# Kernel tuning notes

Hardware: AMD Instinct MI355X
Metric: run time of the kernel (lower is better)

## Reference

```python
import jax, jax.numpy as jnp
import numpy as np

N = 8192
E = 262144
IN_DIM = 128
OUT_DIM = 16


def _linear_params(key, fan_in, fan_out):
    k1, k2 = jax.random.split(key)
    bound = 1.0 / np.sqrt(fan_in)
    W = jax.random.uniform(k1, (fan_in, fan_out), jnp.float32, -bound, bound)
    b = jax.random.uniform(k2, (fan_out,), jnp.float32, -bound, bound)
    return W, b


def setup_inputs() -> dict:
    key = jax.random.key(0)
    ks = jax.random.split(key, 10)
    x = jax.random.normal(ks[0], (N, IN_DIM), jnp.float32)
    edge_index = jax.random.randint(ks[1], (2, E), 0, N, jnp.int64)
    W1, b1 = _linear_params(ks[2], IN_DIM, 128)
    W2, b2 = _linear_params(ks[3], 128, 256)
    W3, b3 = _linear_params(ks[4], 256, 64)
    Wk, bk = _linear_params(ks[5], 256, 256)
    Wq, bq = _linear_params(ks[6], 256, 256)
    Wr, br = _linear_params(ks[7], IN_DIM, 64)
    Wf, bf = _linear_params(ks[8], 64, OUT_DIM)
    ln_g = jnp.ones((64,), jnp.float32)
    ln_b = jnp.zeros((64,), jnp.float32)
    return dict(x=x, edge_index=edge_index, W1=W1, b1=b1, W2=W2, b2=b2,
                W3=W3, b3=b3, Wk=Wk, bk=bk, Wq=Wq, bq=bq, Wr=Wr, br=br,
                ln_g=ln_g, ln_b=ln_b, Wf=Wf, bf=bf)


def gcn_conv(x, W, b, row, col, n):
    # PyG GCNConv: add self-loops, symmetric normalization, aggregate src->dst
    xw = x @ W                                          # [N, F_out]
    loops = jnp.arange(n, dtype=row.dtype)
    r = jnp.concatenate([row, loops])
    c = jnp.concatenate([col, loops])
    deg = jax.ops.segment_sum(jnp.ones_like(c, jnp.float32), c, num_segments=n)
    dinv = jnp.where(deg > 0, jax.lax.rsqrt(jnp.maximum(deg, 1e-12)), 0.0)
    norm = dinv[r] * dinv[c]                            # [E+N]
    out = jax.ops.segment_sum(norm[:, None] * xw[r], c, num_segments=n)
    return out + b


def _forward(x, edge_index, W1, b1, W2, b2, W3, b3, Wk, bk, Wq, bq,
             Wr, br, ln_g, ln_b, Wf, bf):
    row, col = edge_index[0], edge_index[1]
    n = x.shape[0]
    residual = x @ Wr + br                              # [N, 64]
    h = jax.nn.leaky_relu(gcn_conv(x, W1, b1, row, col, n))   # dropout = eval no-op
    h = jax.nn.leaky_relu(gcn_conv(h, W2, b2, row, col, n))   # [N, 256]
    keys = h @ Wk + bk
    queries = h @ Wq + bq
    scores = queries @ keys.T                           # [N, N] dense, as in source
    mask = jnp.zeros((n, n), jnp.float32).at[row, col].set(1.0)
    scores = scores * mask                              # multiplicative mask (faithful)
    attn = jax.nn.softmax(scores, axis=-1)
    h = attn @ h                                        # [N, 256]
    h = jax.nn.leaky_relu(gcn_conv(h, W3, b3, row, col, n))   # [N, 64]
    z = h + residual
    mu = jnp.mean(z, axis=-1, keepdims=True)
    var = jnp.mean((z - mu) ** 2, axis=-1, keepdims=True)
    z = (z - mu) * jax.lax.rsqrt(var + 1e-5) * ln_g + ln_b
    pooled = jnp.max(z, axis=0)                         # 'max' pooling -> [64]
    return pooled @ Wf + bf                             # [OUT_DIM]


def reference(x, edge_index, W1, b1, W2, b2, W3, b3, Wk, bk, Wq, bq,
              Wr, br, ln_g, ln_b, Wf, bf):
    return _forward(x, edge_index, W1, b1, W2, b2, W3, b3, Wk, bk, Wq, bq,
                    Wr, br, ln_g, ln_b, Wf, bf)
```

## Files before the change

kernel.cpp:

```cpp
#include <hip/hip_runtime.h>
#include <hip/hip_fp16.h>
#include <cstdint>
#include <cstddef>

#define NNODES 8192
#define NEDGES 262144
#define MAXDEG 96
#define SMEM_BYTES 10496

typedef _Float16 f16x8 __attribute__((ext_vector_type(8)));
typedef _Float16 h2v   __attribute__((ext_vector_type(2)));
typedef float    f32x4 __attribute__((ext_vector_type(4)));

__device__ __forceinline__ float leaky(float v){ return v > 0.f ? v : 0.01f*v; }

__device__ __forceinline__ unsigned fmap(float f){
  unsigned u = __float_as_uint(f);
  return (u & 0x80000000u) ? ~u : (u | 0x80000000u);
}
__device__ __forceinline__ float funmap(unsigned u){
  return (u & 0x80000000u) ? __uint_as_float(u & 0x7FFFFFFFu) : __uint_as_float(~u);
}
__device__ __forceinline__ h2v as_h2(unsigned u){
  union{ unsigned x; h2v h; } c; c.x = u; return c.h;
}

struct GP {
  const float *x; const int *ei;
  const float *W1,*b1,*W2,*b2,*W3,*b3,*Wk,*bk,*Wq,*bq,*Wr,*br,*lng,*lnb,*Wf,*bfv;
  float* out;
  __half *xh,*xw1h,*h1h,*h1ah,*h2h,*qth,*gh,*hw3h;
  float *resid,*sw3;
  __half *Wqh,*Wkh,*Wqkt,*Wrt,*W1t,*W2t,*W3t;
  float *bqk,*wb,*s0p;
  int *degc,*degr,*csrc,*csrd;
  unsigned* poolpart;
};

__device__ __forceinline__ void pre_unit(const GP& p, int b, char* smem){
  int t = threadIdx.x;
  if (b < 1024){
    int base = (b*256 + t)*4;
    float4 xv = *(const float4*)(p.x + base);
    uint2 o;
    *(__half2*)&o.x = __floats2half2_rn(xv.x, xv.y);
    *(__half2*)&o.y = __floats2half2_rn(xv.z, xv.w);
    *(uint2*)(p.xh + base) = o;
  } else if (b < 1088){
    int base = ((b-1024)*256 + t)*4;
    float4 v = *(const float4*)(p.Wq + base);
    uint2 o;
    *(__half2*)&o.x = __floats2half2_rn(v.x, v.y);
    *(__half2*)&o.y = __floats2half2_rn(v.z, v.w);
    *(uint2*)(p.Wqh + base) = o;
  } else if (b < 1152){
    int base = ((b-1088)*256 + t)*4;
    float4 v = *(const float4*)(p.Wk + base);
    uint2 o;
    *(__half2*)&o.x = __floats2half2_rn(v.x, v.y);
    *(__half2*)&o.y = __floats2half2_rn(v.z, v.w);
    *(uint2*)(p.Wkh + base) = o;
  } else if (b < 1184){
    int idx = (b-1152)*256 + t;
    int nn = idx >> 7, k = idx & 127;
    p.Wrt[idx] = __float2half(p.Wr[k*64 + nn]);
  } else if (b < 1248){
    int idx = (b-1184)*256 + t;
    int nn = idx >> 7, k = idx & 127;
    p.W1t[idx] = __float2half(p.W1[k*128 + nn]);
  } else if (b < 1376){
    int idx = (b-1248)*256 + t;
    int nn = idx >> 7, k = idx & 127;
    p.W2t[idx] = __float2half(p.W2[k*256 + nn]);
  } else if (b < 1440){
    int idx = (b-1376)*256 + t;
    int nn = idx >> 8, k = idx & 255;
    p.W3t[idx] = __float2half(p.W3[k*64 + nn]);
  } else if (b < 1504){
    int idx = (b-1440)*256 + t;
    if (idx < 8192) p.degc[idx]=0; else p.degr[idx-8192]=0;
  } else if (b < 1520){
    p.poolpart[(b-1504)*256 + t] = 0u;
  } else if (b == 1520){
    if (t < 64) p.sw3[t]=0.f;
  } else {
    int c = b - 1521;
    float* ra = (float*)smem; float* rb = ra + 256; float* rc = rb + 256;
    ra[t] = p.Wk[c*256 + t] * p.bq[t];
    rb[t] = p.Wq[c*256 + t] * p.bk[t];
    if (c == 0) rc[t] = p.bq[t]*p.bk[t];
    __syncthreads();
    for (int off=128; off; off>>=1){
      if (t < off){
        ra[t] += ra[t+off];
        rb[t] += rb[t+off];
        if (c == 0) rc[t] += rc[t+off];
      }
      __syncthreads();
    }
    if (t == 0){
      p.bqk[c] = ra[0];
      p.wb[c]  = rb[0];
      if (c == 0) p.s0p[0] = rc[0];
    }
  }
}

__device__ __forceinline__ void gemm_tile(const __half* __restrict__ A,
    const __half* __restrict__ Bt, const float* __restrict__ bias,
    float* __restrict__ Cf, __half* __restrict__ Ch, float* __restrict__ csum,
    int K, int N, int act, int bx, int by,
    _Float16 (*As)[40], _Float16 (*Bs)[40], float* cs){
  int t = threadIdx.x, w = t>>6, lane = t&63;
  int m0 = bx*64, n0 = by*64;
  int quad = lane>>4, l15 = lane&15;
  int srow = t>>2, soff = (t&3)*8;
  f32x4 acc0 = {0.f,0.f,0.f,0.f}, acc1 = acc0, acc2 = acc0, acc3 = acc0;
  for (int k0 = 0; k0 < K; k0 += 32){
    *(uint4*)&As[srow][soff] = *(const uint4*)(A  + (size_t)(m0+srow)*K + k0 + soff);
    *(uint4*)&Bs[srow][soff] = *(const uint4*)(Bt + (size_t)(n0+srow)*K + k0 + soff);
    __syncthreads();
    f16x8 af = *(const f16x8*)&As[w*16 + l15][quad*8];
    f16x8 b0 = *(const f16x8*)&Bs[ 0 + l15][quad*8];
    f16x8 b1 = *(const f16x8*)&Bs[16 + l15][quad*8];
    f16x8 b2 = *(const f16x8*)&Bs[32 + l15][quad*8];
    f16x8 b3 = *(const f16x8*)&Bs[48 + l15][quad*8];
    acc0 = __builtin_amdgcn_mfma_f32_16x16x32_f16(af, b0, acc0, 0,0,0);
    acc1 = __builtin_amdgcn_mfma_f32_16x16x32_f16(af, b1, acc1, 0,0,0);
    acc2 = __builtin_amdgcn_mfma_f32_16x16x32_f16(af, b2, acc2, 0,0,0);
    acc3 = __builtin_amdgcn_mfma_f32_16x16x32_f16(af, b3, acc3, 0,0,0);
    __syncthreads();
  }
  f32x4 accs[4] = {acc0, acc1, acc2, acc3};
  if (csum){
    if (t < 64) cs[t] = 0.f;
    __syncthreads();
    #pragma unroll
    for (int nt=0; nt<4; ++nt){
      float pp = accs[nt][0]+accs[nt][1]+accs[nt][2]+accs[nt][3];
      atomicAdd(&cs[nt*16 + l15], pp);
    }
    __syncthreads();
    if (t < 64) atomicAdd(&csum[n0 + t], cs[t]);
  }
  #pragma unroll
  for (int nt=0; nt<4; ++nt){
    int col = n0 + nt*16 + l15;
    float bv = bias ? bias[col] : 0.f;
    #pragma unroll
    for (int r=0;r<4;r++){
      int row = m0 + w*16 + quad*4 + r;
      float v = accs[nt][r] + bv;
      if (act) v = leaky(v);
      if (Cf) Cf[(size_t)row*N + col] = v;
      if (Ch) Ch[(size_t)row*N + col] = __float2half(v);
    }
  }
}

template<int INS, int OUTS, int ACT>
__device__ __forceinline__ void agg128w(const __half* __restrict__ in,
    const int* __restrict__ deg, const int* __restrict__ src,
    __half* __restrict__ outp, const float* __restrict__ bias, int i){
  int lane = threadIdx.x & 63;
  int dcc = deg[i];
  float dc = rsqrtf((float)(dcc+1));
  int e0 = i*MAXDEG, e1 = e0 + dcc;
  float2 acc = make_float2(0.f, 0.f);
  for (int eb = e0; eb < e1; eb += 8){
    int m = e1 - eb; if (m > 8) m = 8;
    int r[8];
    #pragma unroll
    for (int u=0;u<8;u++) r[u] = src[(u<m) ? eb+u : eb];
    __half2 hv[8]; float sc[8];
    #pragma unroll
    for (int u=0;u<8;u++){
      hv[u] = *(const __half2*)(in + (size_t)r[u]*128 + lane*2);
      sc[u] = INS ? 1.f : rsqrtf((float)(deg[r[u]]+1));
    }
    #pragma unroll
    for (int u=0;u<8;u++){
      if (u < m){
        float2 h = __half22float2(hv[u]);
        if (INS){ acc.x += h.x; acc.y += h.y; }
        else { acc.x = fmaf(sc[u], h.x, acc.x); acc.y = fmaf(sc[u], h.y, acc.y); }
      }
    }
  }
  float2 self = __half22float2(*(const __half2*)(in + (size_t)i*128 + lane*2));
  float ss = INS ? 1.f : dc;
  float ox = dc*(ss*self.x + acc.x);
  float oy = dc*(ss*self.y + acc.y);
  if (ACT){
    ox = leaky(ox + bias[lane*2]);
    oy = leaky(oy + bias[lane*2+1]);
  }
  if (OUTS){ ox *= dc; oy *= dc; }
  *(__half2*)(outp + (size_t)i*128 + lane*2) = __floats2half2_rn(ox, oy);
}

__device__ __forceinline__ void attn_unit(const GP& p, int u){
  const int n = NNODES;
  int w = threadIdx.x>>6, lane = threadIdx.x&63;
  int i = u*4 + w;
  int fo = lane*4;
  uint2 qtu = *(const uint2*)(p.qth + (size_t)i*256 + fo);
  h2v q0 = as_h2(qtu.x), q1 = as_h2(qtu.y);
  float4 wbv = *(const float4*)(p.wb + fo);
  uint2 hiu  = *(const uint2*)(p.h2h + (size_t)i*256 + fo);
  float2 hia = __half22float2(*(__half2*)&hiu.x);
  float2 hib = __half22float2(*(__half2*)&hiu.y);
  float pv = hia.x*wbv.x + hia.y*wbv.y + hib.x*wbv.z + hib.y*wbv.w;
  #pragma unroll
  for (int mm=32; mm; mm>>=1) pv += __shfl_xor(pv, mm, 64);
  float Ei = __expf(pv + p.s0p[0]);
  int dri = p.degr[i];
  int e0 = i*MAXDEG, e1 = e0 + dri;
  float acc = 0.f, dsum = 0.f;
  for (int eb = e0; eb < e1; eb += 8){
    int m = e1 - eb; if (m > 8) m = 8;
    int j[8];
    #pragma unroll
    for (int u8=0;u8<8;u8++) j[u8] = p.csrd[(u8<m) ? eb+u8 : eb];
    uint2 hv[8]; float gv[8];
    #pragma unroll
    for (int u8=0;u8<8;u8++){
      hv[u8] = *(const uint2*)(p.h2h + (size_t)j[u8]*256 + fo);
      gv[u8] = __half2float(p.gh[(size_t)j[u8]*64 + lane]);
    }
    float d[8];
    #pragma unroll
    for (int u8=0;u8<8;u8++)
      d[u8] = __builtin_amdgcn_fdot2(q1, as_h2(hv[u8].y),
              __builtin_amdgcn_fdot2(q0, as_h2(hv[u8].x), 0.f, false), false);
    #pragma unroll
    for (int mm=32; mm; mm>>=1){
      #pragma unroll
      for (int u8=0;u8<8;u8++) d[u8] += __shfl_xor(d[u8], mm, 64);
    }
    #pragma unroll
    for (int u8=0;u8<8;u8++){
      if (u8 < m){
        float we = Ei * __expf(d[u8]);
        dsum += we;
        acc = fmaf(we - 1.f, gv[u8], acc);
      }
    }
  }
  float inv = 1.0f / ((float)(n - dri) + dsum);
  float di = rsqrtf((float)(p.degc[i]+1));
  p.hw3h[(size_t)i*64 + lane] = __float2half(di * (p.sw3[lane] + acc) * inv);
}

__device__ __forceinline__ void zp_wave(const GP& p, int c){
  int lane = threadIdx.x & 63;
  int dcc = p.degc[c];
  float dc = rsqrtf((float)(dcc+1));
  float acc = 0.f;
  int e0 = c*MAXDEG, e1 = e0 + dcc;
  for (int eb = e0; eb < e1; eb += 8){
    int m = e1 - eb; if (m > 8) m = 8;
    int r[8];
    #pragma unroll
    for (int u=0;u<8;u++) r[u] = p.csrc[(u<m) ? eb+u : eb];
    __half hval[8];
    #pragma unroll
    for (int u=0;u<8;u++) hval[u] = p.hw3h[(size_t)r[u]*64 + lane];
    #pragma unroll
    for (int u=0;u<8;u++)
      if (u < m) acc += __half2float(hval[u]);
  }
  float self = __half2float(p.hw3h[(size_t)c*64 + lane]);
  float v = leaky(dc*(self + acc) + p.b3[lane]) + p.resid[(size_t)c*64 + lane];
  float s = v;
  #pragma unroll
  for (int mm=32; mm; mm>>=1) s += __shfl_xor(s, mm, 64);
  float mu = s * (1.0f/64.0f);
  float d = v - mu;
  float s2 = d*d;
  #pragma unroll
  for (int mm=32; mm; mm>>=1) s2 += __shfl_xor(s2, mm, 64);
  float zv = d * rsqrtf(s2*(1.0f/64.0f) + 1e-5f) * p.lng[lane] + p.lnb[lane];
  atomicMax(&p.poolpart[(c & 63)*64 + lane], fmap(zv));
}

__device__ __forceinline__ void final_unit(const GP& p, char* smem){
  int t = threadIdx.x, f = t & 63, g = t >> 6;
  unsigned (*sm)[64] = (unsigned(*)[64])smem;
  float* pool = (float*)(smem + 1024);
  unsigned mu = 0u;
  for (int b = g; b < 64; b += 4) mu = max(mu, p.poolpart[b*64 + f]);
  sm[g][f] = mu;
  __syncthreads();
  if (g == 0)
    pool[f] = funmap(max(max(sm[0][f],sm[1][f]), max(sm[2][f],sm[3][f])));
  __syncthreads();
  if (t < 16){
    float a = p.bfv[t];
    #pragma unroll
    for (int ff=0; ff<64; ++ff) a = fmaf(pool[ff], p.Wf[ff*16 + t], a);
    p.out[t] = a;
  }
}

__global__ __launch_bounds__(256) void k_pre(GP p){
  __shared__ __align__(16) char smem[SMEM_BYTES];
  pre_unit(p, blockIdx.x, smem);
}

__global__ __launch_bounds__(256) void k_sc(GP p){
  __shared__ __align__(16) char smem[SMEM_BYTES];
  _Float16 (*As)[40] = (_Float16(*)[40])smem;
  _Float16 (*Bs)[40] = (_Float16(*)[40])(smem + 5120);
  int b = blockIdx.x;
  if (b < 1024){
    int e = b*256 + threadIdx.x;
    int r = p.ei[e], c = p.ei[NEDGES+e];
    int p1 = atomicAdd(&p.degc[c],1); p.csrc[c*MAXDEG + p1] = r;
    int p2 = atomicAdd(&p.degr[r],1); p.csrd[r*MAXDEG + p2] = c;
  } else if (b < 1280){
    int bb = b - 1024;
    gemm_tile(p.xh, p.W1t, nullptr, nullptr, p.xw1h, nullptr, 128, 128, 0, bb>>1, bb&1, As, Bs, nullptr);
  } else if (b < 1296){
    int bb = b - 1280;
    gemm_tile(p.Wkh, p.Wqh, nullptr, nullptr, p.Wqkt, nullptr, 256, 256, 0, bb&3, bb>>2, As, Bs, nullptr);
  } else {
    gemm_tile(p.xh, p.Wrt, p.br, p.resid, nullptr, nullptr, 128, 64, 0, b-1296, 0, As, Bs, nullptr);
  }
}

__global__ __launch_bounds__(256) void k_agg0(GP p){
  int i = blockIdx.x*4 + (threadIdx.x>>6);
  agg128w<0,1,1>(p.xw1h, p.degc, p.csrc, p.h1h, p.b1, i);
}
__global__ __launch_bounds__(256) void k_agg1(GP p){
  int i = blockIdx.x*4 + (threadIdx.x>>6);
  agg128w<1,0,0>(p.h1h, p.degc, p.csrc, p.h1ah, nullptr, i);
}

__global__ __launch_bounds__(256) void k_gemm2(GP p){
  __shared__ __align__(16) char smem[SMEM_BYTES];
  _Float16 (*As)[40] = (_Float16(*)[40])smem;
  _Float16 (*Bs)[40] = (_Float16(*)[40])(smem + 5120);
  int b = blockIdx.x;
  gemm_tile(p.h1ah, p.W2t, p.b2, nullptr, p.h2h, nullptr, 128, 256, 1, b>>2, b&3, As, Bs, nullptr);
}

__global__ __launch_bounds__(256) void k_mix2(GP p){
  __shared__ __align__(16) char smem[SMEM_BYTES];
  _Float16 (*As)[40] = (_Float16(*)[40])smem;
  _Float16 (*Bs)[40] = (_Float16(*)[40])(smem + 5120);
  float* cs = (float*)(smem + 10240);
  int b = blockIdx.x;
  if (b < 128) gemm_tile(p.h2h, p.W3t, nullptr, nullptr, p.gh, p.sw3, 256, 64, 0, b, 0, As, Bs, cs);
  else {
    int bb = b - 128;
    gemm_tile(p.h2h, p.Wqkt, p.bqk, nullptr, p.qth, nullptr, 256, 256, 0, bb>>2, bb&3, As, Bs, cs);
  }
}

__global__ __launch_bounds__(256) void k_attn(GP p){ attn_unit(p, blockIdx.x); }

__global__ __launch_bounds__(256) void k_zp(GP p){
  int c = blockIdx.x*4 + (threadIdx.x>>6);
  zp_wave(p, c);
}

__global__ __launch_bounds__(256) void k_final(GP p){
  __shared__ __align__(16) char smem[SMEM_BYTES];
  final_unit(p, smem);
}

extern "C" void kernel_launch(void* const* d_in, const int* in_sizes, int n_in,
                              void* d_out, int out_size, void* d_ws, size_t ws_size,
                              hipStream_t stream){
  const int n = NNODES, E = NEDGES;
  char* ws = (char*)d_ws; size_t off = 0;
  auto alloc = [&](size_t bytes)->void*{
    void* pp = ws + off; off += (bytes + 255) & ~(size_t)255; return pp;
  };
  GP p;
  p.x   = (const float*)d_in[0];
  p.ei  = (const int*)d_in[1];
  p.W1  = (const float*)d_in[2];  p.b1 = (const float*)d_in[3];
  p.W2  = (const float*)d_in[4];  p.b2 = (const float*)d_in[5];
  p.W3  = (const float*)d_in[6];  p.b3 = (const float*)d_in[7];
  p.Wk  = (const float*)d_in[8];  p.bk = (const float*)d_in[9];
  p.Wq  = (const float*)d_in[10]; p.bq = (const float*)d_in[11];
  p.Wr  = (const float*)d_in[12]; p.br = (const float*)d_in[13];
  p.lng = (const float*)d_in[14]; p.lnb = (const float*)d_in[15];
  p.Wf  = (const float*)d_in[16]; p.bfv = (const float*)d_in[17];
  p.out = (float*)d_out;

  p.xh   = (__half*)alloc((size_t)n*128*2);
  p.xw1h = (__half*)alloc((size_t)n*128*2);
  p.h1h  = (__half*)alloc((size_t)n*128*2);
  p.h1ah = (__half*)alloc((size_t)n*128*2);
  p.h2h  = (__half*)alloc((size_t)n*256*2);
  p.qth  = (__half*)alloc((size_t)n*256*2);
  p.gh   = (__half*)alloc((size_t)n*64*2);
  p.hw3h = (__half*)alloc((size_t)n*64*2);
  p.resid= (float*)alloc((size_t)n*64*4);
  p.sw3  = (float*)alloc(64*4);
  p.Wqh  = (__half*)alloc(256*256*2);
  p.Wkh  = (__half*)alloc(256*256*2);
  p.Wqkt = (__half*)alloc(256*256*2);
  p.Wrt  = (__half*)alloc(128*64*2);
  p.W1t  = (__half*)alloc(128*128*2);
  p.W2t  = (__half*)alloc(128*256*2);
  p.W3t  = (__half*)alloc(256*64*2);
  p.bqk  = (float*)alloc(256*4);
  p.wb   = (float*)alloc(256*4);
  p.s0p  = (float*)alloc(4);
  p.degc = (int*)alloc((size_t)n*4);
  p.degr = (int*)alloc((size_t)n*4);
  p.csrc = (int*)alloc((size_t)n*MAXDEG*4);
  p.csrd = (int*)alloc((size_t)n*MAXDEG*4);
  p.poolpart = (unsigned*)alloc(64*64*4);

  k_pre  <<<dim3(1777), 256, 0, stream>>>(p);
  k_sc   <<<dim3(1424), 256, 0, stream>>>(p);
  k_agg0 <<<dim3(n/4),  256, 0, stream>>>(p);
  k_agg1 <<<dim3(n/4),  256, 0, stream>>>(p);
  k_gemm2<<<dim3(512),  256, 0, stream>>>(p);
  k_mix2 <<<dim3(640),  256, 0, stream>>>(p);
  k_attn <<<dim3(n/4),  256, 0, stream>>>(p);
  k_zp   <<<dim3(n/4),  256, 0, stream>>>(p);
  k_final<<<dim3(1),    256, 0, stream>>>(p);
}
```

Baseline: 216.7 us.

## Fuse final pooling into zp kernel via last-block counter; transpose attention reductions

Removes the separate single-block final kernel launch by having the last-finishing block of the zp kernel, detected with an atomic done counter, run the pooling and output projection. It reads pool partials via atomics for coherence. The attention edge loop now uses a butterfly transpose reduction, so each lane ends up holding one edge's score and computes a single exp instead of eight. The weights are then broadcast with shuffles. This trades fewer shuffles and exps for extra select logic and a fence-plus-atomic per block.

```diff
diff --git a/kernel.cpp b/kernel.cpp
--- a/kernel.cpp
+++ b/kernel.cpp
@@ -34,7 +34,7 @@
   __half *Wqh,*Wkh,*Wqkt,*Wrt,*W1t,*W2t,*W3t;
   float *bqk,*wb,*s0p;
   int *degc,*degr,*csrc,*csrd;
-  unsigned* poolpart;
+  unsigned* poolpart; unsigned* donecnt;
 };
 
 __device__ __forceinline__ void pre_unit(const GP& p, int b, char* smem){
@@ -83,6 +83,7 @@
     p.poolpart[(b-1504)*256 + t] = 0u;
   } else if (b == 1520){
     if (t < 64) p.sw3[t]=0.f;
+    else if (t == 64) *p.donecnt = 0u;
   } else {
     int c = b - 1521;
     float* ra = (float*)smem; float* rb = ra + 256; float* rc = rb + 256;
@@ -213,10 +214,11 @@
   float pv = hia.x*wbv.x + hia.y*wbv.y + hib.x*wbv.z + hib.y*wbv.w;
   #pragma unroll
   for (int mm=32; mm; mm>>=1) pv += __shfl_xor(pv, mm, 64);
-  float Ei = __expf(pv + p.s0p[0]);
+  float base = pv + p.s0p[0];
   int dri = p.degr[i];
   int e0 = i*MAXDEG, e1 = e0 + dri;
   float acc = 0.f, dsum = 0.f;
+  int slot = lane & 7;
   for (int eb = e0; eb < e1; eb += 8){
     int m = e1 - eb; if (m > 8) m = 8;
     int j[8];
@@ -234,16 +236,31 @@
       d[u8] = __builtin_amdgcn_fdot2(q1, as_h2(hv[u8].y),
               __builtin_amdgcn_fdot2(q0, as_h2(hv[u8].x), 0.f, false), false);
     #pragma unroll
-    for (int mm=32; mm; mm>>=1){
-      #pragma unroll
-      for (int u8=0;u8<8;u8++) d[u8] += __shfl_xor(d[u8], mm, 64);
-    }
+    for (int v=0;v<8;v++) d[v] += __shfl_xor(d[v], 1, 64);
+    float e0_ = (lane&1) ? d[1] : d[0];
+    float e1_ = (lane&1) ? d[3] : d[2];
+    float e2_ = (lane&1) ? d[5] : d[4];
+    float e3_ = (lane&1) ? d[7] : d[6];
+    e0_ += __shfl_xor(e0_, 2, 64);  e1_ += __shfl_xor(e1_, 2, 64);
+    e2_ += __shfl_xor(e2_, 2, 64);  e3_ += __shfl_xor(e3_, 2, 64);
+    float f0_ = (lane&2) ? e1_ : e0_;
+    float f1_ = (lane&2) ? e3_ : e2_;
+    f0_ += __shfl_xor(f0_, 4, 64);  f1_ += __shfl_xor(f1_, 4, 64);
+    float g_ = (lane&4) ? f1_ : f0_;
+    g_ += __shfl_xor(g_,  8, 64);
+    g_ += __shfl_xor(g_, 16, 64);
+    g_ += __shfl_xor(g_, 32, 64);
+    float wep = __expf(g_ + base);
+    float wm = (slot < m) ? wep : 0.f;
+    wm += __shfl_xor(wm, 1, 64);
+    wm += __shfl_xor(wm, 2, 64);
+    wm += __shfl_xor(wm, 4, 64);
+    dsum += wm;
     #pragma unroll
     for (int u8=0;u8<8;u8++){
       if (u8 < m){
-        float we = Ei * __expf(d[u8]);
-        dsum += we;
-        acc = fmaf(we - 1.f, gv[u8], acc);
+        float wu = __shfl(wep, u8, 64);
+        acc = fmaf(wu - 1.f, gv[u8], acc);
       }
     }
   }
@@ -289,7 +306,8 @@
   unsigned (*sm)[64] = (unsigned(*)[64])smem;
   float* pool = (float*)(smem + 1024);
   unsigned mu = 0u;
-  for (int b = g; b < 64; b += 4) mu = max(mu, p.poolpart[b*64 + f]);
+  for (int b = g; b < 64; b += 4)
+    mu = max(mu, atomicOr(&p.poolpart[b*64 + f], 0u));
   sm[g][f] = mu;
   __syncthreads();
   if (g == 0)
@@ -361,14 +379,18 @@
 
 __global__ __launch_bounds__(256) void k_attn(GP p){ attn_unit(p, blockIdx.x); }
 
-__global__ __launch_bounds__(256) void k_zp(GP p){
+__global__ __launch_bounds__(256) void k_zpf(GP p){
+  __shared__ __align__(16) char smem[SMEM_BYTES];
+  __shared__ int lastflag;
   int c = blockIdx.x*4 + (threadIdx.x>>6);
   zp_wave(p, c);
-}
-
-__global__ __launch_bounds__(256) void k_final(GP p){
-  __shared__ __align__(16) char smem[SMEM_BYTES];
-  final_unit(p, smem);
+  if (threadIdx.x == 0){
+    __threadfence();
+    unsigned old = atomicAdd(p.donecnt, 1u);
+    lastflag = (old == (unsigned)(NNODES/4 - 1));
+  }
+  __syncthreads();
+  if (lastflag) final_unit(p, smem);
 }
 
 extern "C" void kernel_launch(void* const* d_in, const int* in_sizes, int n_in,
@@ -417,6 +439,7 @@
   p.csrc = (int*)alloc((size_t)n*MAXDEG*4);
   p.csrd = (int*)alloc((size_t)n*MAXDEG*4);
   p.poolpart = (unsigned*)alloc(64*64*4);
+  p.donecnt  = (unsigned*)alloc(4);
 
   k_pre  <<<dim3(1777), 256, 0, stream>>>(p);
   k_sc   <<<dim3(1424), 256, 0, stream>>>(p);
@@ -425,6 +448,5 @@
   k_gemm2<<<dim3(512),  256, 0, stream>>>(p);
   k_mix2 <<<dim3(640),  256, 0, stream>>>(p);
   k_attn <<<dim3(n/4),  256, 0, stream>>>(p);
-  k_zp   <<<dim3(n/4),  256, 0, stream>>>(p);
-  k_final<<<dim3(1),    256, 0, stream>>>(p);
-}
+  k_zpf  <<<dim3(n/4),  256, 0, stream>>>(p);
+}
```

New measurement: 252.5 us. +16.5%, slower.
